# Performance work log

Hardware: AMD Instinct MI355X
Metric: run time of the kernel (lower is better)

The kernel has to match this reference:

```python
import itertools
import jax, jax.numpy as jnp
import numpy as np

IN_CHANNELS = 8
IN_KERNELS = 32
ORDER = 2


def make_weight(in_channels: int, order: int, in_kernels: int) -> jnp.ndarray:
    """Binary selection weight of shape (Kernels, Combinations, Channels).

    Row r of the (Comb, C) map has 1s at the channels of the r-th combination,
    stacked for all combination sizes 1..order, then repeated per kernel.
    Mirrors torch.combinations + scatter construction in _initialize_weights.
    """
    rows = []
    for o in range(1, order + 1):
        for comb in itertools.combinations(range(in_channels), o):
            row = np.zeros(in_channels, dtype=np.float32)
            row[list(comb)] = 1.0
            rows.append(row)
    w = np.stack(rows, axis=0)  # (Comb, C)
    w = np.broadcast_to(w[None], (in_kernels,) + w.shape).copy()  # (K, Comb, C)
    return jnp.asarray(w)


def setup_inputs() -> dict:
    key = jax.random.key(0)
    B, K, C, T = 8, IN_KERNELS, IN_CHANNELS, 512
    x = jax.random.normal(key, (B, K, C, T), dtype=jnp.float32)
    weight = make_weight(IN_CHANNELS, ORDER, IN_KERNELS)
    return {"x": x, "weight": weight}


def reference(x, weight):
    # x: (B, K, C, T); weight: (K, Comb, C) binary selection map.
    # Multiplicative channel mix: broadcast-mul then replace structural zeros
    # (and any exact data zeros, as in the original) with 1 and take the
    # product over the channel axis.
    y = x[:, :, None, :, :] * weight[None, :, :, :, None]  # (B, K, Comb, C, T)
    y = jnp.where(y != 0, y, jnp.float32(1.0))
    return jnp.prod(y, axis=-2)  # (B, K, Comb, T)
```

## Files before the change

### kernel.cpp

```cpp
#include <hip/hip_runtime.h>


#define CDIM 8
#define TDIM 512
#define COMB 36
#define TQ (TDIM / 4)
#define ITEMS (COMB * TQ)

__device__ __constant__ unsigned char PA[28] = {
    0,0,0,0,0,0,0, 1,1,1,1,1,1, 2,2,2,2,2, 3,3,3,3, 4,4,4, 5,5, 6};
__device__ __constant__ unsigned char PB[28] = {
    1,2,3,4,5,6,7, 2,3,4,5,6,7, 3,4,5,6,7, 4,5,6,7, 5,6,7, 6,7, 7};

__device__ __forceinline__ float4 fix1(float4 v) {
    v.x = (v.x != 0.0f) ? v.x : 1.0f;
    v.y = (v.y != 0.0f) ? v.y : 1.0f;
    v.z = (v.z != 0.0f) ? v.z : 1.0f;
    v.w = (v.w != 0.0f) ? v.w : 1.0f;
    return v;
}

__global__ __launch_bounds__(256) void channelmix_kernel(
    const float* __restrict__ x, float* __restrict__ out) {
    const int bk = blockIdx.y;
    const int item = blockIdx.x * 256 + threadIdx.x;
    const int r = item >> 7;
    const int tq = item & (TQ - 1);

    const float4* __restrict__ xin =
        reinterpret_cast<const float4*>(x + (size_t)bk * CDIM * TDIM);

    float4 v;
    if (r < CDIM) {
        v = fix1(xin[r * TQ + tq]);
    } else {
        const int p = r - CDIM;
        const int a = PA[p];
        const int b = PB[p];
        float4 fa = fix1(xin[a * TQ + tq]);
        float4 fb = fix1(xin[b * TQ + tq]);
        v.x = fa.x * fb.x;
        v.y = fa.y * fb.y;
        v.z = fa.z * fb.z;
        v.w = fa.w * fb.w;
    }

    reinterpret_cast<float4*>(out + (size_t)bk * COMB * TDIM)[r * TQ + tq] = v;
}

extern "C" void kernel_launch(void* const* d_in, const int* in_sizes, int n_in,
                              void* d_out, int out_size, void* d_ws, size_t ws_size,
                              hipStream_t stream) {
    const float* x = (const float*)d_in[0];
    float* out = (float*)d_out;

    dim3 grid(ITEMS / 256, 256);
    channelmix_kernel<<<grid, 256, 0, stream>>>(x, out);
}
```

Baseline: 11.48 us.

## Use flat grid-stride loop with four items per thread and nontemporal stores

Replaces the 2D grid of 4608 blocks with a 1D grid of 1152 blocks, where each thread handles four float4 output items spaced one grid-stride apart. Output writes use nontemporal stores so the large write-once output does not pollute the caches. Fewer blocks and more independent loads per thread aim to cut launch and scheduling overhead and improve memory-level parallelism. The cost is per-item integer division to recover the batch-kernel index, and the strided item assignment reduces input reuse within a block.

```diff
diff --git a/kernel.cpp b/kernel.cpp
--- a/kernel.cpp
+++ b/kernel.cpp
@@ -5,14 +5,20 @@
 #define TDIM 512
 #define COMB 36
 #define TQ (TDIM / 4)
-#define ITEMS (COMB * TQ)
+#define SLAB (COMB * TQ)
+#define TOTAL (256 * SLAB)
+#define NBLK 1152
+#define NTHR 256
+#define STRIDE (NBLK * NTHR)
+
+typedef float f32x4 __attribute__((ext_vector_type(4)));
 
 __device__ __constant__ unsigned char PA[28] = {
     0,0,0,0,0,0,0, 1,1,1,1,1,1, 2,2,2,2,2, 3,3,3,3, 4,4,4, 5,5, 6};
 __device__ __constant__ unsigned char PB[28] = {
     1,2,3,4,5,6,7, 2,3,4,5,6,7, 3,4,5,6,7, 4,5,6,7, 5,6,7, 6,7, 7};
 
-__device__ __forceinline__ float4 fix1(float4 v) {
+__device__ __forceinline__ f32x4 fix1(f32x4 v) {
     v.x = (v.x != 0.0f) ? v.x : 1.0f;
     v.y = (v.y != 0.0f) ? v.y : 1.0f;
     v.z = (v.z != 0.0f) ? v.z : 1.0f;
@@ -20,32 +26,33 @@
     return v;
 }
 
-__global__ __launch_bounds__(256) void channelmix_kernel(
+__global__ __launch_bounds__(NTHR) void channelmix_kernel(
     const float* __restrict__ x, float* __restrict__ out) {
-    const int bk = blockIdx.y;
-    const int item = blockIdx.x * 256 + threadIdx.x;
-    const int r = item >> 7;
-    const int tq = item & (TQ - 1);
+    const int idx = blockIdx.x * NTHR + threadIdx.x;
+    const f32x4* __restrict__ x4 = reinterpret_cast<const f32x4*>(x);
+    f32x4* __restrict__ o4 = reinterpret_cast<f32x4*>(out);
 
-    const float4* __restrict__ xin =
-        reinterpret_cast<const float4*>(x + (size_t)bk * CDIM * TDIM);
+#pragma unroll
+    for (int i = 0; i < 4; ++i) {
+        const unsigned item = (unsigned)idx + i * STRIDE;
+        const unsigned bk = item / SLAB;
+        const unsigned rem = item - bk * SLAB;
+        const unsigned r = rem >> 7;
+        const unsigned tq = rem & (TQ - 1);
 
-    float4 v;
-    if (r < CDIM) {
-        v = fix1(xin[r * TQ + tq]);
-    } else {
-        const int p = r - CDIM;
-        const int a = PA[p];
-        const int b = PB[p];
-        float4 fa = fix1(xin[a * TQ + tq]);
-        float4 fb = fix1(xin[b * TQ + tq]);
-        v.x = fa.x * fb.x;
-        v.y = fa.y * fb.y;
-        v.z = fa.z * fb.z;
-        v.w = fa.w * fb.w;
+        const f32x4* __restrict__ xin = x4 + (size_t)bk * (CDIM * TQ);
+
+        f32x4 v;
+        if (r < CDIM) {
+            v = fix1(xin[r * TQ + tq]);
+        } else {
+            const unsigned p = r - CDIM;
+            const f32x4 fa = fix1(xin[PA[p] * TQ + tq]);
+            const f32x4 fb = fix1(xin[PB[p] * TQ + tq]);
+            v = fa * fb;
+        }
+        __builtin_nontemporal_store(v, o4 + item);
     }
-
-    reinterpret_cast<float4*>(out + (size_t)bk * COMB * TDIM)[r * TQ + tq] = v;
 }
 
 extern "C" void kernel_launch(void* const* d_in, const int* in_sizes, int n_in,
@@ -54,6 +61,5 @@
     const float* x = (const float*)d_in[0];
     float* out = (float*)d_out;
 
-    dim3 grid(ITEMS / 256, 256);
-    channelmix_kernel<<<grid, 256, 0, stream>>>(x, out);
+    channelmix_kernel<<<NBLK, NTHR, 0, stream>>>(x, out);
 }
```

After: 9.524 us. 1.21x faster.
